# Kernel optimization log

Hardware: AMD Instinct MI355X
Metric: run time of the kernel (lower is better)

## Reference

```python
import jax, jax.numpy as jnp
import numpy as np

ALPHA = 0.2   # LeakyReLU negative slope
NEG_INF = -9e15

def setup_inputs() -> dict:
    key = jax.random.key(0)
    k1, k2, k3, k4, k5 = jax.random.split(key, 5)
    B, N, F_IN, F_OUT = 8, 2048, 128, 128
    input = jax.random.normal(k1, (B, N, F_IN), dtype=jnp.float32)
    adj = jax.random.randint(k2, (B, N, N), 0, 2, dtype=jnp.int32)
    W = jax.random.normal(k3, (F_OUT, F_IN), dtype=jnp.float32) * (1.0 / np.sqrt(F_IN))
    a_src = jax.random.normal(k4, (F_OUT, 1), dtype=jnp.float32) * 0.1
    a_dst = jax.random.normal(k5, (F_OUT, 1), dtype=jnp.float32) * 0.1
    return {"input": input, "adj": adj, "W": W, "a_src": a_src, "a_dst": a_dst}

def reference(input, adj, W, a_src, a_dst):
    # h = input @ W^T : [B,N,F_out]
    h = jnp.einsum('bnf,of->bno', input, W)
    src = h @ a_src              # [B,N,1]
    dst = h @ a_dst              # [B,N,1]
    e = src + jnp.swapaxes(dst, 1, 2)          # [B,N,N] additive scores
    e = jnp.where(e > 0, e, ALPHA * e)         # LeakyReLU
    att = jnp.where(adj > 0, e, NEG_INF)
    att = jax.nn.softmax(att, axis=2)
    # dropout is identity in eval mode
    h_prime = jnp.einsum('bnm,bmo->bno', att, h)
    return jax.nn.elu(h_prime)                 # concat=True path
```

## Files before the change

### kernel.cpp

```cpp
#include <hip/hip_runtime.h>
#include <stdint.h>

#define NB 8
#define NN 2048
#define FF 128
#define ALPHA 0.2f

typedef unsigned short u16;
typedef __attribute__((ext_vector_type(8))) short bf16x8;
typedef __attribute__((ext_vector_type(4))) float f32x4;

__device__ __forceinline__ float bf2f(u16 h) {
    union { uint32_t u; float f; } v; v.u = ((uint32_t)h) << 16; return v.f;
}
__device__ __forceinline__ u16 f2bf(float x) {
    union { float f; uint32_t u; } v; v.f = x;
    uint32_t r = v.u + 0x7fffu + ((v.u >> 16) & 1u);
    return (u16)(r >> 16);
}
__device__ __forceinline__ uint4 pack8(const float o[8]) {
    uint4 r;
    r.x = (uint32_t)f2bf(o[0]) | ((uint32_t)f2bf(o[1]) << 16);
    r.y = (uint32_t)f2bf(o[2]) | ((uint32_t)f2bf(o[3]) << 16);
    r.z = (uint32_t)f2bf(o[4]) | ((uint32_t)f2bf(o[5]) << 16);
    r.w = (uint32_t)f2bf(o[6]) | ((uint32_t)f2bf(o[7]) << 16);
    return r;
}
__device__ __forceinline__ void load8f(const float* p, size_t i, float o[8]) {
    float4 a = *(const float4*)(p + i);
    float4 b = *(const float4*)(p + i + 4);
    o[0]=a.x; o[1]=a.y; o[2]=a.z; o[3]=a.w;
    o[4]=b.x; o[5]=b.y; o[6]=b.z; o[7]=b.w;
}

__global__ __launch_bounds__(256) void k_prep(
    const float* __restrict__ x,
    const float* __restrict__ w,
    const float* __restrict__ as_,
    const float* __restrict__ ad_,
    u16* __restrict__ hT,
    float* __restrict__ srcp, float* __restrict__ dstp)
{
    __shared__ __attribute__((aligned(16))) u16 Ws[128][136];
    __shared__ __attribute__((aligned(16))) u16 Xs[64][136];
    __shared__ float waS[128], waD[128];
    __shared__ float lredS[64][4], lredD[64][4];

    const int b  = blockIdx.x >> 5;
    const int n0 = (blockIdx.x & 31) * 64;
    const int t  = threadIdx.x;
    const int wv = t >> 6, lane = t & 63, quad = lane >> 4, lr = lane & 15;

    {
        const int o = t >> 1, fb = (t & 1) * 64;
        #pragma unroll
        for (int k = 0; k < 8; ++k) {
            float v8[8];
            load8f(w, (size_t)o * FF + fb + k * 8, v8);
            *(uint4*)&Ws[o][fb + k * 8] = pack8(v8);
        }
    }
    if (t < 128) {
        float s = 0.f;
        for (int o = 0; o < FF; ++o) s += w[(size_t)o * FF + t] * as_[o];
        waS[t] = s;
    } else {
        const int f = t - 128;
        float s = 0.f;
        for (int o = 0; o < FF; ++o) s += w[(size_t)o * FF + f] * ad_[o];
        waD[f] = s;
    }
    __syncthreads();

    {
        const int r = t >> 2, q = t & 3;
        float sp = 0.f, dp = 0.f;
        #pragma unroll
        for (int k = 0; k < 4; ++k) {
            float v8[8];
            load8f(x, (size_t)(b * NN + n0 + r) * FF + q * 32 + k * 8, v8);
            *(uint4*)&Xs[r][q * 32 + k * 8] = pack8(v8);
            #pragma unroll
            for (int u = 0; u < 8; ++u) {
                sp += v8[u] * waS[q * 32 + k * 8 + u];
                dp += v8[u] * waD[q * 32 + k * 8 + u];
            }
        }
        lredS[r][q] = sp; lredD[r][q] = dp;
    }
    __syncthreads();
    if (t < 64) {
        srcp[b * NN + n0 + t] = lredS[t][0] + lredS[t][1] + lredS[t][2] + lredS[t][3];
        dstp[b * NN + n0 + t] = lredD[t][0] + lredD[t][1] + lredD[t][2] + lredD[t][3];
    }

    f32x4 hacc[8] = {};
    #pragma unroll
    for (int kc = 0; kc < 4; ++kc) {
        const int ko = kc * 32 + quad * 8;
        bf16x8 a = *(const bf16x8*)&Xs[wv * 16 + lr][ko];
        #pragma unroll
        for (int t8 = 0; t8 < 8; ++t8) {
            bf16x8 bb = *(const bf16x8*)&Ws[t8 * 16 + lr][ko];
            hacc[t8] = __builtin_amdgcn_mfma_f32_16x16x32_bf16(a, bb, hacc[t8], 0, 0, 0);
        }
    }
    __syncthreads();

    u16* HsB = &Ws[0][0];
    #pragma unroll
    for (int t8 = 0; t8 < 8; ++t8) {
        #pragma unroll
        for (int reg = 0; reg < 4; ++reg)
            HsB[(t8 * 16 + lr) * 68 + wv * 16 + quad * 4 + reg] = f2bf(hacc[t8][reg]);
    }
    __syncthreads();
    {
        const int r16 = t >> 4, ng = t & 15;
        #pragma unroll
        for (int s = 0; s < 8; ++s) {
            const int o = s * 16 + r16;
            uint2 v = *(const uint2*)&HsB[o * 68 + ng * 4];
            *(uint2*)&hT[(size_t)(b * FF + o) * NN + n0 + ng * 4] = v;
        }
    }
}

__global__ __launch_bounds__(256) void k_attn(
    const int*   __restrict__ adj,
    const u16*   __restrict__ hT,
    const float* __restrict__ srcp,
    const float* __restrict__ dstp,
    float* __restrict__ out)
{
    __shared__ __attribute__((aligned(16))) u16 Hs[128][136];
    __shared__ __attribute__((aligned(16))) u16 Ps[32][136];
    __shared__ float lred[32][8];
    __shared__ float lrow[32];

    const int b  = blockIdx.x >> 6;
    const int i0 = (blockIdx.x & 63) * 32;
    const int t  = threadIdx.x;
    const int wv = t >> 6, lane = t & 63, quad = lane >> 4, lr = lane & 15;
    const int rowt = (wv & 1) * 16, colt = (wv >> 1) * 64;

    const int il = t >> 3, q = t & 7;
    const float src_i  = srcp[b * NN + i0 + il];
    const int*   adjrow = adj + (size_t)(b * NN + i0 + il) * NN;
    const float* dstb   = dstp + b * NN;

    const int r16 = t >> 4, c16 = t & 15;

    f32x4 acc[4] = {};
    float lacc = 0.f;

    for (int j0 = 0; j0 < NN; j0 += 128) {
        #pragma unroll
        for (int s = 0; s < 8; ++s) {
            const int o = s * 16 + r16;
            uint4 v = *(const uint4*)(hT + (size_t)(b * FF + o) * NN + j0 + c16 * 8);
            *(uint4*)&Hs[o][c16 * 8] = v;
        }
        {
            int4   a4[4]; float4 d4[4];
            #pragma unroll
            for (int it = 0; it < 4; ++it) {
                a4[it] = *(const int4*)(adjrow + j0 + q * 16 + it * 4);
                d4[it] = *(const float4*)(dstb + j0 + q * 16 + it * 4);
            }
            u16 pb[16];
            #pragma unroll
            for (int it = 0; it < 4; ++it) {
                const int*   ai = (const int*)&a4[it];
                const float* dv = (const float*)&d4[it];
                #pragma unroll
                for (int u = 0; u < 4; ++u) {
                    float e = src_i + dv[u];
                    e = e > 0.f ? e : ALPHA * e;
                    float p = __expf(e);
                    p = (ai[u] > 0) ? p : 0.f;
                    const u16 pv = f2bf(p);
                    pb[it * 4 + u] = pv;
                    lacc += bf2f(pv);
                }
            }
            uint4 w0, w1;
            w0.x = (uint32_t)pb[0]  | ((uint32_t)pb[1]  << 16);
            w0.y = (uint32_t)pb[2]  | ((uint32_t)pb[3]  << 16);
            w0.z = (uint32_t)pb[4]  | ((uint32_t)pb[5]  << 16);
            w0.w = (uint32_t)pb[6]  | ((uint32_t)pb[7]  << 16);
            w1.x = (uint32_t)pb[8]  | ((uint32_t)pb[9]  << 16);
            w1.y = (uint32_t)pb[10] | ((uint32_t)pb[11] << 16);
            w1.z = (uint32_t)pb[12] | ((uint32_t)pb[13] << 16);
            w1.w = (uint32_t)pb[14] | ((uint32_t)pb[15] << 16);
            *(uint4*)&Ps[il][q * 16]     = w0;
            *(uint4*)&Ps[il][q * 16 + 8] = w1;
        }
        __syncthreads();

        #pragma unroll
        for (int kc = 0; kc < 4; ++kc) {
            const int ko = kc * 32 + quad * 8;
            bf16x8 a = *(const bf16x8*)&Ps[rowt + lr][ko];
            #pragma unroll
            for (int t8 = 0; t8 < 4; ++t8) {
                bf16x8 bb = *(const bf16x8*)&Hs[colt + t8 * 16 + lr][ko];
                acc[t8] = __builtin_amdgcn_mfma_f32_16x16x32_bf16(a, bb, acc[t8], 0, 0, 0);
            }
        }
        __syncthreads();
    }

    lred[il][q] = lacc;
    __syncthreads();
    if (t < 32) {
        float s = 0.f;
        #pragma unroll
        for (int k = 0; k < 8; ++k) s += lred[t][k];
        lrow[t] = s;
    }
    __syncthreads();

    #pragma unroll
    for (int t8 = 0; t8 < 4; ++t8) {
        const int col = colt + t8 * 16 + lr;
        #pragma unroll
        for (int reg = 0; reg < 4; ++reg) {
            const int row = rowt + quad * 4 + reg;
            const float l = fmaxf(lrow[row], 1e-30f);
            float v = acc[t8][reg] / l;
            v = v > 0.f ? v : __expf(v) - 1.f;
            out[(size_t)(b * NN + i0 + row) * FF + col] = v;
        }
    }
}

extern "C" void kernel_launch(void* const* d_in, const int* in_sizes, int n_in,
                              void* d_out, int out_size, void* d_ws, size_t ws_size,
                              hipStream_t stream) {
    const float* x = nullptr; const int* adj = nullptr; const float* w = nullptr;
    const float* as_ = nullptr; const float* ad_ = nullptr;
    for (int i = 0; i < n_in; ++i) {
        const long long s = in_sizes[i];
        if      (s == (long long)NB * NN * FF)  x   = (const float*)d_in[i];
        else if (s == (long long)NB * NN * NN)  adj = (const int*)d_in[i];
        else if (s == FF * FF)                  w   = (const float*)d_in[i];
        else if (s == FF) { if (!as_) as_ = (const float*)d_in[i]; else ad_ = (const float*)d_in[i]; }
    }
    if (!x)   x   = (const float*)d_in[0];
    if (!adj) adj = (const int*)d_in[1];
    if (!w)   w   = (const float*)d_in[2];
    if (!as_) as_ = (const float*)d_in[3];
    if (!ad_) ad_ = (const float*)d_in[4];
    float* out = (float*)d_out;

    u16*   hT   = (u16*)d_ws;
    float* srcp = (float*)((char*)d_ws + (size_t)NB * FF * NN * sizeof(u16));
    float* dstp = srcp + NB * NN;

    k_prep<<<256, 256, 0, stream>>>(x, w, as_, ad_, hT, srcp, dstp);
    k_attn<<<512, 256, 0, stream>>>(adj, hT, srcp, dstp, out);
}
```

Before: 221.1 us.

## Stream H tiles from global, double-buffer P and prefetch adjacency registers

The attention kernel no longer stages hT tiles in shared memory. MFMA B-operands are read directly from global memory (relying on L2/cache reuse), and the probability tile is double-buffered in LDS so one barrier per iteration suffices. The whole dst vector is preloaded into LDS, and the next adjacency chunk is prefetched into registers to overlap the global loads with the exp/MFMA work, with launch bounds requesting 2 blocks per CU. The risk is that uncoalesced, strided global reads of hT (stride NN per row) cost more than the LDS staging did.

```diff
diff --git a/kernel.cpp b/kernel.cpp
--- a/kernel.cpp
+++ b/kernel.cpp
@@ -126,15 +126,15 @@
     }
 }
 
-__global__ __launch_bounds__(256) void k_attn(
+__global__ __launch_bounds__(256, 2) void k_attn(
     const int*   __restrict__ adj,
     const u16*   __restrict__ hT,
     const float* __restrict__ srcp,
     const float* __restrict__ dstp,
     float* __restrict__ out)
 {
-    __shared__ __attribute__((aligned(16))) u16 Hs[128][136];
-    __shared__ __attribute__((aligned(16))) u16 Ps[32][136];
+    __shared__ __attribute__((aligned(16))) u16 Ps[2][32][136];
+    __shared__ __attribute__((aligned(16))) float dstAll[2048];
     __shared__ float lred[32][8];
     __shared__ float lrow[32];
 
@@ -146,69 +146,75 @@
 
     const int il = t >> 3, q = t & 7;
     const float src_i  = srcp[b * NN + i0 + il];
-    const int*   adjrow = adj + (size_t)(b * NN + i0 + il) * NN;
-    const float* dstb   = dstp + b * NN;
-
-    const int r16 = t >> 4, c16 = t & 15;
+    const int*  adjrow = adj + (size_t)(b * NN + i0 + il) * NN;
+    const u16*  hTb    = hT + (size_t)b * FF * NN;
+
+    {
+        const float* dp = dstp + b * NN;
+        *(float4*)&dstAll[t * 8]     = *(const float4*)(dp + t * 8);
+        *(float4*)&dstAll[t * 8 + 4] = *(const float4*)(dp + t * 8 + 4);
+    }
+    int4 areg[2][4];
+    #pragma unroll
+    for (int it = 0; it < 4; ++it)
+        areg[0][it] = *(const int4*)(adjrow + q * 16 + it * 4);
+    __syncthreads();
 
     f32x4 acc[4] = {};
     float lacc = 0.f;
 
-    for (int j0 = 0; j0 < NN; j0 += 128) {
-        #pragma unroll
-        for (int s = 0; s < 8; ++s) {
-            const int o = s * 16 + r16;
-            uint4 v = *(const uint4*)(hT + (size_t)(b * FF + o) * NN + j0 + c16 * 8);
-            *(uint4*)&Hs[o][c16 * 8] = v;
-        }
-        {
-            int4   a4[4]; float4 d4[4];
-            #pragma unroll
-            for (int it = 0; it < 4; ++it) {
-                a4[it] = *(const int4*)(adjrow + j0 + q * 16 + it * 4);
-                d4[it] = *(const float4*)(dstb + j0 + q * 16 + it * 4);
+    for (int k = 0; k < 16; ++k) {
+        const int j0 = k << 7, pb = k & 1;
+
+        if (k < 15) {
+            #pragma unroll
+            for (int it = 0; it < 4; ++it)
+                areg[pb ^ 1][it] = *(const int4*)(adjrow + j0 + 128 + q * 16 + it * 4);
+        }
+
+        u16 pv16[16];
+        #pragma unroll
+        for (int it = 0; it < 4; ++it) {
+            const int4 a4 = areg[pb][it];
+            const int* ai = (const int*)&a4;
+            float4 d4 = *(const float4*)&dstAll[j0 + q * 16 + it * 4];
+            const float* dv = (const float*)&d4;
+            #pragma unroll
+            for (int u = 0; u < 4; ++u) {
+                float e = src_i + dv[u];
+                e = e > 0.f ? e : ALPHA * e;
+                float p = __expf(e);
+                p = (ai[u] > 0) ? p : 0.f;
+                const u16 pvb = f2bf(p);
+                pv16[it * 4 + u] = pvb;
+                lacc += bf2f(pvb);
             }
-            u16 pb[16];
-            #pragma unroll
-            for (int it = 0; it < 4; ++it) {
-                const int*   ai = (const int*)&a4[it];
-                const float* dv = (const float*)&d4[it];
-                #pragma unroll
-                for (int u = 0; u < 4; ++u) {
-                    float e = src_i + dv[u];
-                    e = e > 0.f ? e : ALPHA * e;
-                    float p = __expf(e);
-                    p = (ai[u] > 0) ? p : 0.f;
-                    const u16 pv = f2bf(p);
-                    pb[it * 4 + u] = pv;
-                    lacc += bf2f(pv);
-                }
-            }
-            uint4 w0, w1;
-            w0.x = (uint32_t)pb[0]  | ((uint32_t)pb[1]  << 16);
-            w0.y = (uint32_t)pb[2]  | ((uint32_t)pb[3]  << 16);
-            w0.z = (uint32_t)pb[4]  | ((uint32_t)pb[5]  << 16);
-            w0.w = (uint32_t)pb[6]  | ((uint32_t)pb[7]  << 16);
-            w1.x = (uint32_t)pb[8]  | ((uint32_t)pb[9]  << 16);
-            w1.y = (uint32_t)pb[10] | ((uint32_t)pb[11] << 16);
-            w1.z = (uint32_t)pb[12] | ((uint32_t)pb[13] << 16);
-            w1.w = (uint32_t)pb[14] | ((uint32_t)pb[15] << 16);
-            *(uint4*)&Ps[il][q * 16]     = w0;
-            *(uint4*)&Ps[il][q * 16 + 8] = w1;
-        }
+        }
+        uint4 w0, w1;
+        w0.x = (uint32_t)pv16[0]  | ((uint32_t)pv16[1]  << 16);
+        w0.y = (uint32_t)pv16[2]  | ((uint32_t)pv16[3]  << 16);
+        w0.z = (uint32_t)pv16[4]  | ((uint32_t)pv16[5]  << 16);
+        w0.w = (uint32_t)pv16[6]  | ((uint32_t)pv16[7]  << 16);
+        w1.x = (uint32_t)pv16[8]  | ((uint32_t)pv16[9]  << 16);
+        w1.y = (uint32_t)pv16[10] | ((uint32_t)pv16[11] << 16);
+        w1.z = (uint32_t)pv16[12] | ((uint32_t)pv16[13] << 16);
+        w1.w = (uint32_t)pv16[14] | ((uint32_t)pv16[15] << 16);
+        *(uint4*)&Ps[pb][il][q * 16]     = w0;
+        *(uint4*)&Ps[pb][il][q * 16 + 8] = w1;
+
         __syncthreads();
 
+        const u16* hTj = hTb + j0;
         #pragma unroll
         for (int kc = 0; kc < 4; ++kc) {
             const int ko = kc * 32 + quad * 8;
-            bf16x8 a = *(const bf16x8*)&Ps[rowt + lr][ko];
+            bf16x8 a = *(const bf16x8*)&Ps[pb][rowt + lr][ko];
             #pragma unroll
             for (int t8 = 0; t8 < 4; ++t8) {
-                bf16x8 bb = *(const bf16x8*)&Hs[colt + t8 * 16 + lr][ko];
+                bf16x8 bb = *(const bf16x8*)(hTj + (size_t)(colt + t8 * 16 + lr) * NN + ko);
                 acc[t8] = __builtin_amdgcn_mfma_f32_16x16x32_bf16(a, bb, acc[t8], 0, 0, 0);
             }
         }
-        __syncthreads();
     }
 
     lred[il][q] = lacc;
@@ -216,7 +222,7 @@
     if (t < 32) {
         float s = 0.f;
         #pragma unroll
-        for (int k = 0; k < 8; ++k) s += lred[t][k];
+        for (int kk = 0; kk < 8; ++kk) s += lred[t][kk];
         lrow[t] = s;
     }
     __syncthreads();
```

Result: slower. 305.5 us (+38.1%).

## Split key range across waves and build MFMA fragments in registers

Applied to the files above, without the earlier changes.

Rewrites the attention kernel so each block handles 16 rows, and each of its four waves covers a disjoint quarter of the key dimension. Probabilities are computed directly into MFMA A-fragments in registers, and B-fragments are loaded straight from global hT, so the per-tile shared-memory staging and the two barriers per iteration are gone. Partial accumulators and denominators are reduced across waves through shared memory once at the end, with vectorized output stores. The grid doubles and launch bounds request 4 blocks per SM. In exchange, hT is re-read from global/L2 by more blocks, and the B loads are strided gathers rather than coalesced tile loads.

```diff
diff --git a/kernel.cpp b/kernel.cpp
--- a/kernel.cpp
+++ b/kernel.cpp
@@ -126,112 +126,105 @@
     }
 }
 
-__global__ __launch_bounds__(256) void k_attn(
+__global__ __launch_bounds__(256, 4) void k_attn(
     const int*   __restrict__ adj,
     const u16*   __restrict__ hT,
     const float* __restrict__ srcp,
     const float* __restrict__ dstp,
     float* __restrict__ out)
 {
-    __shared__ __attribute__((aligned(16))) u16 Hs[128][136];
-    __shared__ __attribute__((aligned(16))) u16 Ps[32][136];
-    __shared__ float lred[32][8];
-    __shared__ float lrow[32];
-
-    const int b  = blockIdx.x >> 6;
-    const int i0 = (blockIdx.x & 63) * 32;
+    __shared__ __attribute__((aligned(16))) float accL[4][16][132];
+    __shared__ float denL[4][16];
+
+    const int b  = blockIdx.x >> 7;
+    const int i0 = (blockIdx.x & 127) * 16;
     const int t  = threadIdx.x;
     const int wv = t >> 6, lane = t & 63, quad = lane >> 4, lr = lane & 15;
-    const int rowt = (wv & 1) * 16, colt = (wv >> 1) * 64;
-
-    const int il = t >> 3, q = t & 7;
-    const float src_i  = srcp[b * NN + i0 + il];
-    const int*   adjrow = adj + (size_t)(b * NN + i0 + il) * NN;
-    const float* dstb   = dstp + b * NN;
-
-    const int r16 = t >> 4, c16 = t & 15;
-
-    f32x4 acc[4] = {};
+
+    const int*   adjrow = adj + (size_t)(b * NN + i0 + lr) * NN;
+    const float* dstb   = dstp + (size_t)b * NN;
+    const u16*   hTb    = hT + (size_t)b * FF * NN;
+    const float  src_i  = srcp[b * NN + i0 + lr];
+
+    f32x4 acc[8] = {};
     float lacc = 0.f;
 
-    for (int j0 = 0; j0 < NN; j0 += 128) {
-        #pragma unroll
-        for (int s = 0; s < 8; ++s) {
-            const int o = s * 16 + r16;
-            uint4 v = *(const uint4*)(hT + (size_t)(b * FF + o) * NN + j0 + c16 * 8);
-            *(uint4*)&Hs[o][c16 * 8] = v;
-        }
-        {
-            int4   a4[4]; float4 d4[4];
-            #pragma unroll
-            for (int it = 0; it < 4; ++it) {
-                a4[it] = *(const int4*)(adjrow + j0 + q * 16 + it * 4);
-                d4[it] = *(const float4*)(dstb + j0 + q * 16 + it * 4);
-            }
-            u16 pb[16];
-            #pragma unroll
-            for (int it = 0; it < 4; ++it) {
-                const int*   ai = (const int*)&a4[it];
-                const float* dv = (const float*)&d4[it];
-                #pragma unroll
-                for (int u = 0; u < 4; ++u) {
-                    float e = src_i + dv[u];
-                    e = e > 0.f ? e : ALPHA * e;
-                    float p = __expf(e);
-                    p = (ai[u] > 0) ? p : 0.f;
-                    const u16 pv = f2bf(p);
-                    pb[it * 4 + u] = pv;
-                    lacc += bf2f(pv);
-                }
-            }
-            uint4 w0, w1;
-            w0.x = (uint32_t)pb[0]  | ((uint32_t)pb[1]  << 16);
-            w0.y = (uint32_t)pb[2]  | ((uint32_t)pb[3]  << 16);
-            w0.z = (uint32_t)pb[4]  | ((uint32_t)pb[5]  << 16);
-            w0.w = (uint32_t)pb[6]  | ((uint32_t)pb[7]  << 16);
-            w1.x = (uint32_t)pb[8]  | ((uint32_t)pb[9]  << 16);
-            w1.y = (uint32_t)pb[10] | ((uint32_t)pb[11] << 16);
-            w1.z = (uint32_t)pb[12] | ((uint32_t)pb[13] << 16);
-            w1.w = (uint32_t)pb[14] | ((uint32_t)pb[15] << 16);
-            *(uint4*)&Ps[il][q * 16]     = w0;
-            *(uint4*)&Ps[il][q * 16 + 8] = w1;
-        }
-        __syncthreads();
-
+    #pragma unroll
+    for (int kit = 0; kit < 4; ++kit) {
+        const int j0 = (wv + 4 * kit) << 7;
         #pragma unroll
         for (int kc = 0; kc < 4; ++kc) {
-            const int ko = kc * 32 + quad * 8;
-            bf16x8 a = *(const bf16x8*)&Ps[rowt + lr][ko];
-            #pragma unroll
-            for (int t8 = 0; t8 < 4; ++t8) {
-                bf16x8 bb = *(const bf16x8*)&Hs[colt + t8 * 16 + lr][ko];
-                acc[t8] = __builtin_amdgcn_mfma_f32_16x16x32_bf16(a, bb, acc[t8], 0, 0, 0);
-            }
-        }
-        __syncthreads();
-    }
-
-    lred[il][q] = lacc;
-    __syncthreads();
-    if (t < 32) {
-        float s = 0.f;
-        #pragma unroll
-        for (int k = 0; k < 8; ++k) s += lred[t][k];
-        lrow[t] = s;
-    }
-    __syncthreads();
-
-    #pragma unroll
-    for (int t8 = 0; t8 < 4; ++t8) {
-        const int col = colt + t8 * 16 + lr;
-        #pragma unroll
-        for (int reg = 0; reg < 4; ++reg) {
-            const int row = rowt + quad * 4 + reg;
-            const float l = fmaxf(lrow[row], 1e-30f);
-            float v = acc[t8][reg] / l;
-            v = v > 0.f ? v : __expf(v) - 1.f;
-            out[(size_t)(b * NN + i0 + row) * FF + col] = v;
-        }
+            const int jk = j0 + kc * 32 + quad * 8;
+            int4   a0 = *(const int4*)(adjrow + jk);
+            int4   a1 = *(const int4*)(adjrow + jk + 4);
+            float4 d0 = *(const float4*)(dstb + jk);
+            float4 d1 = *(const float4*)(dstb + jk + 4);
+            const int*   ai0 = (const int*)&a0;
+            const int*   ai1 = (const int*)&a1;
+            const float* dv0 = (const float*)&d0;
+            const float* dv1 = (const float*)&d1;
+            union { bf16x8 v; u16 h[8]; uint32_t w32[4]; } frag;
+            #pragma unroll
+            for (int u = 0; u < 4; ++u) {
+                float e = src_i + dv0[u];
+                e = e > 0.f ? e : ALPHA * e;
+                float p = __expf(e);
+                p = (ai0[u] > 0) ? p : 0.f;
+                const u16 pv = f2bf(p);
+                frag.h[u] = pv;
+                lacc += bf2f(pv);
+            }
+            #pragma unroll
+            for (int u = 0; u < 4; ++u) {
+                float e = src_i + dv1[u];
+                e = e > 0.f ? e : ALPHA * e;
+                float p = __expf(e);
+                p = (ai1[u] > 0) ? p : 0.f;
+                const u16 pv = f2bf(p);
+                frag.h[4 + u] = pv;
+                lacc += bf2f(pv);
+            }
+            #pragma unroll
+            for (int t8 = 0; t8 < 8; ++t8) {
+                bf16x8 bb = *(const bf16x8*)(hTb + (size_t)(t8 * 16 + lr) * NN + jk);
+                acc[t8] = __builtin_amdgcn_mfma_f32_16x16x32_bf16(frag.v, bb, acc[t8], 0, 0, 0);
+            }
+        }
+    }
+
+    lacc += __shfl_xor(lacc, 16, 64);
+    lacc += __shfl_xor(lacc, 32, 64);
+    if (quad == 0) denL[wv][lr] = lacc;
+
+    #pragma unroll
+    for (int t8 = 0; t8 < 8; ++t8) {
+        #pragma unroll
+        for (int reg = 0; reg < 4; ++reg)
+            accL[wv][quad * 4 + reg][t8 * 16 + lr] = acc[t8][reg];
+    }
+    __syncthreads();
+
+    {
+        const int r = t >> 4, g = t & 15;
+        float den = denL[0][r] + denL[1][r] + denL[2][r] + denL[3][r];
+        den = fmaxf(den, 1e-30f);
+        float n[8] = {};
+        #pragma unroll
+        for (int w8 = 0; w8 < 4; ++w8) {
+            float4 p0 = *(const float4*)&accL[w8][r][g * 8];
+            float4 p1 = *(const float4*)&accL[w8][r][g * 8 + 4];
+            n[0] += p0.x; n[1] += p0.y; n[2] += p0.z; n[3] += p0.w;
+            n[4] += p1.x; n[5] += p1.y; n[6] += p1.z; n[7] += p1.w;
+        }
+        float* op = out + ((size_t)(b * NN + i0 + r) * FF + g * 8);
+        float o8[8];
+        #pragma unroll
+        for (int u = 0; u < 8; ++u) {
+            float v = n[u] / den;
+            o8[u] = v > 0.f ? v : __expf(v) - 1.f;
+        }
+        *(float4*)op       = make_float4(o8[0], o8[1], o8[2], o8[3]);
+        *(float4*)(op + 4) = make_float4(o8[4], o8[5], o8[6], o8[7]);
     }
 }
 
@@ -259,5 +252,5 @@
     float* dstp = srcp + NB * NN;
 
     k_prep<<<256, 256, 0, stream>>>(x, w, as_, ad_, hT, srcp, dstp);
-    k_attn<<<512, 256, 0, stream>>>(adj, hT, srcp, dstp, out);
-}
+    k_attn<<<1024, 256, 0, stream>>>(adj, hT, srcp, dstp, out);
+}
```

Result: slower. 292.3 us (+32.2%).
